# Kernel optimization log

Hardware: AMD Instinct MI355X
Metric: run time of the kernel (lower is better)

Reference implementation:

```python
import jax, jax.numpy as jnp
import numpy as np

N = 8192      # reg_num == number of nodes
E = 524288    # number of edges
OUT = 32      # out_num


def gcn_conv(x, src, dst, W, b, n):
    """PyG GCNConv: add self-loops, symmetric deg^-1/2 normalization, linear, scatter-add, bias."""
    loop = jnp.arange(n)
    s = jnp.concatenate([src, loop])
    d = jnp.concatenate([dst, loop])
    deg = jax.ops.segment_sum(jnp.ones(s.shape, dtype=x.dtype), d, num_segments=n)
    dinv = jnp.where(deg > 0, jax.lax.rsqrt(deg), jnp.zeros_like(deg))
    norm = dinv[s] * dinv[d]                      # [E+N]
    h = x @ W.T                                    # [N, out_ch]
    out = jax.ops.segment_sum(norm[:, None] * h[s], d, num_segments=n)
    return out + b


def setup_inputs() -> dict:
    key = jax.random.key(0)
    ks = jax.random.split(key, 12)
    data = jax.random.normal(ks[0], (N, 2), dtype=jnp.float32)
    edge = jax.random.randint(ks[1], (2, E), 0, N, dtype=jnp.int64)
    # GCNConv weights (PyG Linear: y = x @ W.T, bias added after aggregation)
    W1 = jax.random.normal(ks[2], (4, 2), dtype=jnp.float32) * 0.5
    b1 = jnp.zeros((4,), dtype=jnp.float32)
    W2 = jax.random.normal(ks[3], (2, 4), dtype=jnp.float32) * 0.5
    b2 = jnp.zeros((2,), dtype=jnp.float32)
    W3 = jax.random.normal(ks[4], (1, 2), dtype=jnp.float32) * 0.5
    b3 = jnp.zeros((1,), dtype=jnp.float32)
    # trailing MLP: Linear(N, 2N) -> Tanh -> Linear(2N, OUT) -> Tanh
    Wa = jax.random.normal(ks[5], (2 * N, N), dtype=jnp.float32) * (1.0 / np.sqrt(N))
    ba = jnp.zeros((2 * N,), dtype=jnp.float32)
    Wb = jax.random.normal(ks[6], (OUT, 2 * N), dtype=jnp.float32) * (1.0 / np.sqrt(2 * N))
    bb = jnp.zeros((OUT,), dtype=jnp.float32)
    return {"data": data, "edge": edge, "W1": W1, "b1": b1, "W2": W2, "b2": b2,
            "W3": W3, "b3": b3, "Wa": Wa, "ba": ba, "Wb": Wb, "bb": bb}


def reference(data, edge, W1, b1, W2, b2, W3, b3, Wa, ba, Wb, bb):
    src, dst = edge[0], edge[1]
    n = data.shape[0]
    out = jax.nn.relu(gcn_conv(data, src, dst, W1, b1, n))
    out = jax.nn.relu(gcn_conv(out, src, dst, W2, b2, n))
    out = gcn_conv(out, src, dst, W3, b3, n)       # [N, 1]
    out = out.reshape(1, -1)                        # [1, N]
    out = jnp.tanh(out @ Wa.T + ba)                 # [1, 2N]
    out = jnp.tanh(out @ Wb.T + bb)                 # [1, OUT]
    return out
```

## Files before the change

kernel.cpp:

```cpp
#include <hip/hip_runtime.h>
#include <hip/hip_bf16.h>

#define NN   8192
#define NE   524288
#define DH   16384
#define NOUT 32

typedef float f32x4 __attribute__((ext_vector_type(4)));


__global__ __launch_bounds__(256) void k_deg_acc(const int* __restrict__ dst, float* degacc) {
    int e = blockIdx.x * blockDim.x + threadIdx.x;
    if (e < NE) atomicAdd(&degacc[dst[e]], 1.0f);
}

__global__ __launch_bounds__(256) void k_dinv_h1(const float* __restrict__ x0,
                                                 const float* __restrict__ W1,
                                                 float* dinv, float* h1) {
    int i = blockIdx.x * blockDim.x + threadIdx.x;
    if (i >= NN) return;
    dinv[i] = rsqrtf(dinv[i] + 1.0f);
    float a = x0[2 * i], b = x0[2 * i + 1];
    f32x4 h;
#pragma unroll
    for (int c = 0; c < 4; ++c) h[c] = a * W1[2 * c] + b * W1[2 * c + 1];
    *(f32x4*)(h1 + 4 * i) = h;
}

__global__ __launch_bounds__(256) void k_scat4(const int* __restrict__ src,
                                               const int* __restrict__ dst,
                                               const float* __restrict__ dinv,
                                               const float* __restrict__ h,
                                               float* agg) {
    int e = blockIdx.x * blockDim.x + threadIdx.x;
    if (e >= NE) return;
    int s = src[e], d = dst[e];
    float nrm = dinv[s] * dinv[d];
    float4 hv = *(const float4*)(h + 4 * s);
    atomicAdd(&agg[4 * d + 0], nrm * hv.x);
    atomicAdd(&agg[4 * d + 1], nrm * hv.y);
    atomicAdd(&agg[4 * d + 2], nrm * hv.z);
    atomicAdd(&agg[4 * d + 3], nrm * hv.w);
}

__global__ __launch_bounds__(256) void k_fin1_h2(const float* __restrict__ dinv,
                                                 const float* __restrict__ h1,
                                                 const float* __restrict__ agg1,
                                                 const float* __restrict__ b1,
                                                 const float* __restrict__ W2,
                                                 float* h2) {
    int i = blockIdx.x * blockDim.x + threadIdx.x;
    if (i >= NN) return;
    float di2 = dinv[i] * dinv[i];
    float x1[4];
#pragma unroll
    for (int c = 0; c < 4; ++c) {
        float t = agg1[4 * i + c] + di2 * h1[4 * i + c] + b1[c];
        x1[c] = fmaxf(t, 0.0f);
    }
#pragma unroll
    for (int c = 0; c < 2; ++c) {
        float t = 0.0f;
#pragma unroll
        for (int k = 0; k < 4; ++k) t += x1[k] * W2[4 * c + k];
        h2[2 * i + c] = t;
    }
}

__global__ __launch_bounds__(256) void k_scat2(const int* __restrict__ src,
                                               const int* __restrict__ dst,
                                               const float* __restrict__ dinv,
                                               const float* __restrict__ h,
                                               float* agg) {
    int e = blockIdx.x * blockDim.x + threadIdx.x;
    if (e >= NE) return;
    int s = src[e], d = dst[e];
    float nrm = dinv[s] * dinv[d];
    float2 hv = *(const float2*)(h + 2 * s);
    atomicAdd(&agg[2 * d + 0], nrm * hv.x);
    atomicAdd(&agg[2 * d + 1], nrm * hv.y);
}

__global__ __launch_bounds__(256) void k_fin2_h3(const float* __restrict__ dinv,
                                                 const float* __restrict__ h2,
                                                 const float* __restrict__ agg2,
                                                 const float* __restrict__ b2,
                                                 const float* __restrict__ W3,
                                                 float* h3) {
    int i = blockIdx.x * blockDim.x + threadIdx.x;
    if (i >= NN) return;
    float di2 = dinv[i] * dinv[i];
    float x2a = fmaxf(agg2[2 * i + 0] + di2 * h2[2 * i + 0] + b2[0], 0.0f);
    float x2b = fmaxf(agg2[2 * i + 1] + di2 * h2[2 * i + 1] + b2[1], 0.0f);
    h3[i] = x2a * W3[0] + x2b * W3[1];
}

__global__ __launch_bounds__(256) void k_scat1(const int* __restrict__ src,
                                               const int* __restrict__ dst,
                                               const float* __restrict__ dinv,
                                               const float* __restrict__ h,
                                               float* agg) {
    int e = blockIdx.x * blockDim.x + threadIdx.x;
    if (e >= NE) return;
    int s = src[e], d = dst[e];
    atomicAdd(&agg[d], dinv[s] * dinv[d] * h[s]);
}

__global__ __launch_bounds__(256) void k_fin3(const float* __restrict__ dinv,
                                              const float* __restrict__ h3,
                                              const float* __restrict__ agg3,
                                              const float* __restrict__ b3,
                                              float* v) {
    int i = blockIdx.x * blockDim.x + threadIdx.x;
    if (i >= NN) return;
    v[i] = agg3[i] + dinv[i] * dinv[i] * h3[i] + b3[0];
}


__global__ __launch_bounds__(256) void k_mv1(const float* __restrict__ v,
                                             const float* __restrict__ Wa,
                                             const float* __restrict__ ba,
                                             float* __restrict__ y) {
    int wid  = threadIdx.x >> 6;
    int lane = threadIdx.x & 63;
    int j = blockIdx.x * 4 + wid;
    const f32x4* wr = (const f32x4*)(Wa + (size_t)j * NN);
    const f32x4* vv = (const f32x4*)v;
    float acc = 0.0f;
#pragma unroll 8
    for (int it = 0; it < (NN / 4) / 64; ++it) {
        int idx = it * 64 + lane;
        f32x4 w = __builtin_nontemporal_load(&wr[idx]);
        f32x4 x = vv[idx];
        acc += w.x * x.x + w.y * x.y + w.z * x.z + w.w * x.w;
    }
#pragma unroll
    for (int off = 32; off > 0; off >>= 1) acc += __shfl_down(acc, off, 64);
    if (lane == 0) y[j] = tanhf(acc + ba[j]);
}

__global__ __launch_bounds__(256) void k_mv2(const float* __restrict__ y,
                                             const float* __restrict__ Wb,
                                             const float* __restrict__ bb,
                                             float* __restrict__ out) {
    int wid  = threadIdx.x >> 6;
    int lane = threadIdx.x & 63;
    int o = blockIdx.x * 4 + wid;
    const f32x4* wr = (const f32x4*)(Wb + (size_t)o * DH);
    const f32x4* yy = (const f32x4*)y;
    float acc = 0.0f;
#pragma unroll 8
    for (int it = 0; it < (DH / 4) / 64; ++it) {
        int idx = it * 64 + lane;
        f32x4 w = wr[idx];
        f32x4 x = yy[idx];
        acc += w.x * x.x + w.y * x.y + w.z * x.z + w.w * x.w;
    }
#pragma unroll
    for (int off = 32; off > 0; off >>= 1) acc += __shfl_down(acc, off, 64);
    if (lane == 0) out[o] = tanhf(acc + bb[o]);
}


extern "C" void kernel_launch(void* const* d_in, const int* in_sizes, int n_in,
                              void* d_out, int out_size, void* d_ws, size_t ws_size,
                              hipStream_t stream) {
    const float* data = (const float*)d_in[0];
    const int*   edge = (const int*)d_in[1];
    const float* W1   = (const float*)d_in[2];
    const float* b1   = (const float*)d_in[3];
    const float* W2   = (const float*)d_in[4];
    const float* b2   = (const float*)d_in[5];
    const float* W3   = (const float*)d_in[6];
    const float* b3   = (const float*)d_in[7];
    const float* Wa   = (const float*)d_in[8];
    const float* ba   = (const float*)d_in[9];
    const float* Wb   = (const float*)d_in[10];
    const float* bb   = (const float*)d_in[11];
    float* out = (float*)d_out;

    const int* src = edge;
    const int* dst = edge + NE;

    float* ws   = (float*)d_ws;
    float* dinv = ws;
    float* agg1 = dinv + NN;
    float* agg2 = agg1 + NN * 4;
    float* agg3 = agg2 + NN * 2;
    float* h1   = agg3 + NN;
    float* h2   = h1 + NN * 4;
    float* h3   = h2 + NN * 2;
    float* v    = h3 + NN;
    float* y1   = v + NN;

    dim3 blk(256);
    dim3 gN((NN + 255) / 256);
    dim3 gE((NE + 255) / 256);

    hipMemsetAsync(dinv, 0, (size_t)(NN * 8) * sizeof(float), stream);

    k_deg_acc<<<gE, blk, 0, stream>>>(dst, dinv);
    k_dinv_h1<<<gN, blk, 0, stream>>>(data, W1, dinv, h1);
    k_scat4<<<gE, blk, 0, stream>>>(src, dst, dinv, h1, agg1);
    k_fin1_h2<<<gN, blk, 0, stream>>>(dinv, h1, agg1, b1, W2, h2);
    k_scat2<<<gE, blk, 0, stream>>>(src, dst, dinv, h2, agg2);
    k_fin2_h3<<<gN, blk, 0, stream>>>(dinv, h2, agg2, b2, W3, h3);
    k_scat1<<<gE, blk, 0, stream>>>(src, dst, dinv, h3, agg3);
    k_fin3<<<gN, blk, 0, stream>>>(dinv, h3, agg3, b3, v);
    k_mv1<<<dim3(DH / 4), blk, 0, stream>>>(v, Wa, ba, y1);
    k_mv2<<<dim3(NOUT / 4), blk, 0, stream>>>(y1, Wb, bb, out);
}
```

Before: 894.3 us.

## Build CSR by destination and replace atomic scatters with wave-per-node gathers

Replaces the three per-edge float atomic scatter passes with a one-time CSR build: an integer histogram, a single-block scan that also computes dinv, and a cursor-based bucket fill of source indices. Each GCN layer then becomes a wavefront-per-node gather with a shuffle reduction, and the finalize/ReLU/next-linear step is fused into the gather kernel. This cuts the number of float atomics and finalize launches, at the cost of a serial single-block scan, an atomic build pass and irregular gathers with load imbalance across nodes.

```diff
diff --git a/kernel.cpp b/kernel.cpp
--- a/kernel.cpp
+++ b/kernel.cpp
@@ -9,17 +9,56 @@
 typedef float f32x4 __attribute__((ext_vector_type(4)));
 
 
-__global__ __launch_bounds__(256) void k_deg_acc(const int* __restrict__ dst, float* degacc) {
+__global__ __launch_bounds__(256) void k_hist(const int* __restrict__ dst, int* cnt) {
     int e = blockIdx.x * blockDim.x + threadIdx.x;
-    if (e < NE) atomicAdd(&degacc[dst[e]], 1.0f);
-}
-
-__global__ __launch_bounds__(256) void k_dinv_h1(const float* __restrict__ x0,
-                                                 const float* __restrict__ W1,
-                                                 float* dinv, float* h1) {
+    if (e < NE) atomicAdd(&cnt[dst[e]], 1);
+}
+
+__global__ __launch_bounds__(256) void k_scan(const int* __restrict__ cnt,
+                                              int* __restrict__ row,
+                                              int* __restrict__ cursor,
+                                              float* __restrict__ dinv) {
+    __shared__ int sm[256];
+    int t = threadIdx.x;
+    int base = t * 32;
+    int local[32];
+    int sum = 0;
+#pragma unroll
+    for (int k = 0; k < 32; ++k) { local[k] = cnt[base + k]; sum += local[k]; }
+    sm[t] = sum;
+    __syncthreads();
+    for (int off = 1; off < 256; off <<= 1) {
+        int v = (t >= off) ? sm[t - off] : 0;
+        __syncthreads();
+        sm[t] += v;
+        __syncthreads();
+    }
+    int pre = (t == 0) ? 0 : sm[t - 1];
+#pragma unroll
+    for (int k = 0; k < 32; ++k) {
+        row[base + k] = pre;
+        cursor[base + k] = pre;
+        dinv[base + k] = rsqrtf((float)local[k] + 1.0f);
+        pre += local[k];
+    }
+    if (t == 255) row[NN] = pre;
+}
+
+__global__ __launch_bounds__(256) void k_build(const int* __restrict__ src,
+                                               const int* __restrict__ dst,
+                                               int* __restrict__ cursor,
+                                               int* __restrict__ srcs) {
+    int e = blockIdx.x * blockDim.x + threadIdx.x;
+    if (e >= NE) return;
+    int p = atomicAdd(&cursor[dst[e]], 1);
+    srcs[p] = src[e];
+}
+
+__global__ __launch_bounds__(256) void k_h1(const float* __restrict__ x0,
+                                            const float* __restrict__ W1,
+                                            float* __restrict__ h1) {
     int i = blockIdx.x * blockDim.x + threadIdx.x;
     if (i >= NN) return;
-    dinv[i] = rsqrtf(dinv[i] + 1.0f);
     float a = x0[2 * i], b = x0[2 * i + 1];
     f32x4 h;
 #pragma unroll
@@ -27,93 +66,96 @@
     *(f32x4*)(h1 + 4 * i) = h;
 }
 
-__global__ __launch_bounds__(256) void k_scat4(const int* __restrict__ src,
-                                               const int* __restrict__ dst,
-                                               const float* __restrict__ dinv,
-                                               const float* __restrict__ h,
-                                               float* agg) {
-    int e = blockIdx.x * blockDim.x + threadIdx.x;
-    if (e >= NE) return;
-    int s = src[e], d = dst[e];
-    float nrm = dinv[s] * dinv[d];
-    float4 hv = *(const float4*)(h + 4 * s);
-    atomicAdd(&agg[4 * d + 0], nrm * hv.x);
-    atomicAdd(&agg[4 * d + 1], nrm * hv.y);
-    atomicAdd(&agg[4 * d + 2], nrm * hv.z);
-    atomicAdd(&agg[4 * d + 3], nrm * hv.w);
-}
-
-__global__ __launch_bounds__(256) void k_fin1_h2(const float* __restrict__ dinv,
-                                                 const float* __restrict__ h1,
-                                                 const float* __restrict__ agg1,
-                                                 const float* __restrict__ b1,
-                                                 const float* __restrict__ W2,
-                                                 float* h2) {
-    int i = blockIdx.x * blockDim.x + threadIdx.x;
-    if (i >= NN) return;
-    float di2 = dinv[i] * dinv[i];
-    float x1[4];
-#pragma unroll
-    for (int c = 0; c < 4; ++c) {
-        float t = agg1[4 * i + c] + di2 * h1[4 * i + c] + b1[c];
-        x1[c] = fmaxf(t, 0.0f);
-    }
-#pragma unroll
-    for (int c = 0; c < 2; ++c) {
-        float t = 0.0f;
-#pragma unroll
-        for (int k = 0; k < 4; ++k) t += x1[k] * W2[4 * c + k];
-        h2[2 * i + c] = t;
-    }
-}
-
-__global__ __launch_bounds__(256) void k_scat2(const int* __restrict__ src,
-                                               const int* __restrict__ dst,
-                                               const float* __restrict__ dinv,
-                                               const float* __restrict__ h,
-                                               float* agg) {
-    int e = blockIdx.x * blockDim.x + threadIdx.x;
-    if (e >= NE) return;
-    int s = src[e], d = dst[e];
-    float nrm = dinv[s] * dinv[d];
-    float2 hv = *(const float2*)(h + 2 * s);
-    atomicAdd(&agg[2 * d + 0], nrm * hv.x);
-    atomicAdd(&agg[2 * d + 1], nrm * hv.y);
-}
-
-__global__ __launch_bounds__(256) void k_fin2_h3(const float* __restrict__ dinv,
-                                                 const float* __restrict__ h2,
-                                                 const float* __restrict__ agg2,
-                                                 const float* __restrict__ b2,
-                                                 const float* __restrict__ W3,
-                                                 float* h3) {
-    int i = blockIdx.x * blockDim.x + threadIdx.x;
-    if (i >= NN) return;
-    float di2 = dinv[i] * dinv[i];
-    float x2a = fmaxf(agg2[2 * i + 0] + di2 * h2[2 * i + 0] + b2[0], 0.0f);
-    float x2b = fmaxf(agg2[2 * i + 1] + di2 * h2[2 * i + 1] + b2[1], 0.0f);
-    h3[i] = x2a * W3[0] + x2b * W3[1];
-}
-
-__global__ __launch_bounds__(256) void k_scat1(const int* __restrict__ src,
-                                               const int* __restrict__ dst,
-                                               const float* __restrict__ dinv,
-                                               const float* __restrict__ h,
-                                               float* agg) {
-    int e = blockIdx.x * blockDim.x + threadIdx.x;
-    if (e >= NE) return;
-    int s = src[e], d = dst[e];
-    atomicAdd(&agg[d], dinv[s] * dinv[d] * h[s]);
-}
-
-__global__ __launch_bounds__(256) void k_fin3(const float* __restrict__ dinv,
-                                              const float* __restrict__ h3,
-                                              const float* __restrict__ agg3,
-                                              const float* __restrict__ b3,
-                                              float* v) {
-    int i = blockIdx.x * blockDim.x + threadIdx.x;
-    if (i >= NN) return;
-    v[i] = agg3[i] + dinv[i] * dinv[i] * h3[i] + b3[0];
+
+__global__ __launch_bounds__(256) void k_g4(const int* __restrict__ row,
+                                            const int* __restrict__ srcs,
+                                            const float* __restrict__ dinv,
+                                            const float* __restrict__ h1,
+                                            const float* __restrict__ b1,
+                                            const float* __restrict__ W2,
+                                            float* __restrict__ h2) {
+    int wid = threadIdx.x >> 6, lane = threadIdx.x & 63;
+    int i = blockIdx.x * 4 + wid;
+    int beg = row[i], end = row[i + 1];
+    float a0 = 0, a1 = 0, a2 = 0, a3 = 0;
+    for (int p = beg + lane; p < end; p += 64) {
+        int s = srcs[p];
+        float w = dinv[s];
+        float4 hv = *(const float4*)(h1 + 4 * s);
+        a0 += w * hv.x; a1 += w * hv.y; a2 += w * hv.z; a3 += w * hv.w;
+    }
+#pragma unroll
+    for (int off = 32; off > 0; off >>= 1) {
+        a0 += __shfl_down(a0, off, 64);
+        a1 += __shfl_down(a1, off, 64);
+        a2 += __shfl_down(a2, off, 64);
+        a3 += __shfl_down(a3, off, 64);
+    }
+    if (lane == 0) {
+        float di = dinv[i];
+        float4 hs = *(const float4*)(h1 + 4 * i);
+        float x0v = fmaxf(di * (a0 + di * hs.x) + b1[0], 0.0f);
+        float x1v = fmaxf(di * (a1 + di * hs.y) + b1[1], 0.0f);
+        float x2v = fmaxf(di * (a2 + di * hs.z) + b1[2], 0.0f);
+        float x3v = fmaxf(di * (a3 + di * hs.w) + b1[3], 0.0f);
+        float2 o;
+        o.x = x0v * W2[0] + x1v * W2[1] + x2v * W2[2] + x3v * W2[3];
+        o.y = x0v * W2[4] + x1v * W2[5] + x2v * W2[6] + x3v * W2[7];
+        *(float2*)(h2 + 2 * i) = o;
+    }
+}
+
+__global__ __launch_bounds__(256) void k_g2(const int* __restrict__ row,
+                                            const int* __restrict__ srcs,
+                                            const float* __restrict__ dinv,
+                                            const float* __restrict__ h2,
+                                            const float* __restrict__ b2,
+                                            const float* __restrict__ W3,
+                                            float* __restrict__ h3) {
+    int wid = threadIdx.x >> 6, lane = threadIdx.x & 63;
+    int i = blockIdx.x * 4 + wid;
+    int beg = row[i], end = row[i + 1];
+    float a0 = 0, a1 = 0;
+    for (int p = beg + lane; p < end; p += 64) {
+        int s = srcs[p];
+        float w = dinv[s];
+        float2 hv = *(const float2*)(h2 + 2 * s);
+        a0 += w * hv.x; a1 += w * hv.y;
+    }
+#pragma unroll
+    for (int off = 32; off > 0; off >>= 1) {
+        a0 += __shfl_down(a0, off, 64);
+        a1 += __shfl_down(a1, off, 64);
+    }
+    if (lane == 0) {
+        float di = dinv[i];
+        float2 hs = *(const float2*)(h2 + 2 * i);
+        float x0v = fmaxf(di * (a0 + di * hs.x) + b2[0], 0.0f);
+        float x1v = fmaxf(di * (a1 + di * hs.y) + b2[1], 0.0f);
+        h3[i] = x0v * W3[0] + x1v * W3[1];
+    }
+}
+
+__global__ __launch_bounds__(256) void k_g1(const int* __restrict__ row,
+                                            const int* __restrict__ srcs,
+                                            const float* __restrict__ dinv,
+                                            const float* __restrict__ h3,
+                                            const float* __restrict__ b3,
+                                            float* __restrict__ v) {
+    int wid = threadIdx.x >> 6, lane = threadIdx.x & 63;
+    int i = blockIdx.x * 4 + wid;
+    int beg = row[i], end = row[i + 1];
+    float a0 = 0;
+    for (int p = beg + lane; p < end; p += 64) {
+        int s = srcs[p];
+        a0 += dinv[s] * h3[s];
+    }
+#pragma unroll
+    for (int off = 32; off > 0; off >>= 1) a0 += __shfl_down(a0, off, 64);
+    if (lane == 0) {
+        float di = dinv[i];
+        v[i] = di * (a0 + di * h3[i]) + b3[0];
+    }
 }
 
 
@@ -182,31 +224,32 @@
     const int* src = edge;
     const int* dst = edge + NE;
 
-    float* ws   = (float*)d_ws;
-    float* dinv = ws;
-    float* agg1 = dinv + NN;
-    float* agg2 = agg1 + NN * 4;
-    float* agg3 = agg2 + NN * 2;
-    float* h1   = agg3 + NN;
-    float* h2   = h1 + NN * 4;
-    float* h3   = h2 + NN * 2;
-    float* v    = h3 + NN;
-    float* y1   = v + NN;
+    char* ws = (char*)d_ws;
+    int*   cnt    = (int*)ws;
+    int*   row    = cnt + NN;
+    int*   cursor = row + NN + 1;
+    int*   srcs   = cursor + NN;
+    float* dinv   = (float*)(srcs + NE);
+    float* h1     = dinv + NN;
+    float* h2     = h1 + NN * 4;
+    float* h3     = h2 + NN * 2;
+    float* v      = h3 + NN;
+    float* y1     = v + NN;
 
     dim3 blk(256);
     dim3 gN((NN + 255) / 256);
     dim3 gE((NE + 255) / 256);
-
-    hipMemsetAsync(dinv, 0, (size_t)(NN * 8) * sizeof(float), stream);
-
-    k_deg_acc<<<gE, blk, 0, stream>>>(dst, dinv);
-    k_dinv_h1<<<gN, blk, 0, stream>>>(data, W1, dinv, h1);
-    k_scat4<<<gE, blk, 0, stream>>>(src, dst, dinv, h1, agg1);
-    k_fin1_h2<<<gN, blk, 0, stream>>>(dinv, h1, agg1, b1, W2, h2);
-    k_scat2<<<gE, blk, 0, stream>>>(src, dst, dinv, h2, agg2);
-    k_fin2_h3<<<gN, blk, 0, stream>>>(dinv, h2, agg2, b2, W3, h3);
-    k_scat1<<<gE, blk, 0, stream>>>(src, dst, dinv, h3, agg3);
-    k_fin3<<<gN, blk, 0, stream>>>(dinv, h3, agg3, b3, v);
-    k_mv1<<<dim3(DH / 4), blk, 0, stream>>>(v, Wa, ba, y1);
-    k_mv2<<<dim3(NOUT / 4), blk, 0, stream>>>(y1, Wb, bb, out);
-}
+    dim3 gW(NN / 4);
+
+    hipMemsetAsync(cnt, 0, (size_t)NN * sizeof(int), stream);
+
+    k_hist <<<gE, blk, 0, stream>>>(dst, cnt);
+    k_h1   <<<gN, blk, 0, stream>>>(data, W1, h1);
+    k_scan <<<dim3(1), blk, 0, stream>>>(cnt, row, cursor, dinv);
+    k_build<<<gE, blk, 0, stream>>>(src, dst, cursor, srcs);
+    k_g4   <<<gW, blk, 0, stream>>>(row, srcs, dinv, h1, b1, W2, h2);
+    k_g2   <<<gW, blk, 0, stream>>>(row, srcs, dinv, h2, b2, W3, h3);
+    k_g1   <<<gW, blk, 0, stream>>>(row, srcs, dinv, h3, b3, v);
+    k_mv1  <<<dim3(DH / 4), blk, 0, stream>>>(v, Wa, ba, y1);
+    k_mv2  <<<dim3(NOUT / 4), blk, 0, stream>>>(y1, Wb, bb, out);
+}
```

Measured after the change: 747.6 us. 1.2x faster.
